# Performance work log

Hardware: AMD Instinct MI355X
Metric: run time of the kernel (lower is better)

Reference implementation:

```python
import jax, jax.numpy as jnp
import numpy as np


def conv(x, w, b=None, pad=0):
    y = jax.lax.conv_general_dilated(x, w, (1, 1), [(pad, pad), (pad, pad)],
                                     dimension_numbers=('NCHW', 'OIHW', 'NCHW'))
    if b is not None:
        y = y + b[None, :, None, None]
    return y


def bn(x, g, b, m, v, eps=1e-5):
    scale = g / jnp.sqrt(v + eps)
    return (x - m[None, :, None, None]) * scale[None, :, None, None] + b[None, :, None, None]


def channel_gate(x, w1, b1, w2, b2):
    # avg pool -> MLP -> sigmoid, returns [B, C, 1, 1]
    p = x.mean(axis=(2, 3))                       # [B, C]
    h = jax.nn.relu(p @ w1.T + b1)                # [B, C//r]
    a = h @ w2.T + b2                             # [B, C]
    return jax.nn.sigmoid(a)[:, :, None, None]


def setup_inputs() -> dict:
    key = jax.random.key(0)
    ks = iter(jax.random.split(key, 48))
    B, Cin, H, W = 2, 256, 64, 64
    Ci = Cin // 2          # inter_channels = 128
    Cr = Ci // 16          # gate bottleneck = 8
    def nrm(shape, s=0.05):
        return jax.random.normal(next(ks), shape, jnp.float32) * s
    d = {}
    d['q'] = jax.random.normal(next(ks), (B, Cin, H, W), jnp.float32)
    d['s'] = jax.random.normal(next(ks), (B, Cin, H, W), jnp.float32)
    # Trans_s: conv3x3 + BN
    d['ts_w'] = nrm((Ci, Cin, 3, 3)); d['ts_b'] = jnp.zeros(Ci)
    d['ts_g'] = jnp.ones(Ci); d['ts_be'] = jnp.zeros(Ci)
    d['ts_m'] = nrm((Ci,), 0.01); d['ts_v'] = jnp.ones(Ci)
    # Trans_q: conv3x3 + BN
    d['tq_w'] = nrm((Ci, Cin, 3, 3)); d['tq_b'] = jnp.zeros(Ci)
    d['tq_g'] = jnp.ones(Ci); d['tq_be'] = jnp.zeros(Ci)
    d['tq_m'] = nrm((Ci,), 0.01); d['tq_v'] = jnp.ones(Ci)
    # common_v 1x1
    d['cv_w'] = nrm((Ci, Ci, 1, 1)); d['cv_b'] = jnp.zeros(Ci)
    # key/query 1x1 projections (out = Ci//2)
    d['k1_w'] = nrm((Ci // 2, Ci, 1, 1)); d['k1_b'] = jnp.zeros(Ci // 2)
    d['q1_w'] = nrm((Ci // 2, Ci, 1, 1)); d['q1_b'] = jnp.zeros(Ci // 2)
    d['k2_w'] = nrm((Ci // 2, Ci, 1, 1)); d['k2_b'] = jnp.zeros(Ci // 2)
    d['q2_w'] = nrm((Ci // 2, Ci, 1, 1)); d['q2_b'] = jnp.zeros(Ci // 2)
    # ChannelGate MLP
    d['g1_w'] = nrm((Cr, Ci)); d['g1_b'] = jnp.zeros(Cr)
    d['g2_w'] = nrm((Ci, Cr)); d['g2_b'] = jnp.zeros(Ci)
    # conv_cat: conv3x3 (no bias) + BN
    d['cc_w'] = nrm((Ci, 2 * Ci, 3, 3))
    d['cc_g'] = jnp.ones(Ci); d['cc_be'] = jnp.zeros(Ci)
    d['cc_m'] = nrm((Ci,), 0.01); d['cc_v'] = jnp.ones(Ci)
    return d


def reference(q, s, ts_w, ts_b, ts_g, ts_be, ts_m, ts_v,
              tq_w, tq_b, tq_g, tq_be, tq_m, tq_v,
              cv_w, cv_b, k1_w, k1_b, q1_w, q1_b, k2_w, k2_b, q2_w, q2_b,
              g1_w, g1_b, g2_w, g2_b, cc_w, cc_g, cc_be, cc_m, cc_v):
    # stems: conv3x3 + BN + ReLU
    s = jax.nn.relu(bn(conv(s, ts_w, ts_b, pad=1), ts_g, ts_be, ts_m, ts_v))
    q = jax.nn.relu(bn(conv(q, tq_w, tq_b, pad=1), tq_g, tq_be, tq_m, tq_v))
    B, C, H, W = q.shape
    N = H * W
    # values
    v_q1 = conv(q, cv_w, cv_b)                          # [B,C,H,W]
    v_s1 = conv(s, cv_w, cv_b)
    v_q = v_q1.reshape(B, C, N).transpose(0, 2, 1)      # [B,N,C]
    v_s = v_s1.reshape(B, C, N).transpose(0, 2, 1)
    # dual keys / queries with negation trick
    k1 = conv(s, k1_w, k1_b).reshape(B, C // 2, N)
    k2 = conv(q, k2_w, k2_b).reshape(B, C // 2, N)
    key_cat = jnp.concatenate([k1, -k2], axis=1).transpose(0, 2, 1)   # [B,N,C]
    q1x = conv(s, q1_w, q1_b).reshape(B, C // 2, N)
    q2x = conv(q, q2_w, q2_b).reshape(B, C // 2, N)
    query_cat = jnp.concatenate([q1x, q2x], axis=1)                    # [B,C,N]
    # abs-score attention, dual softmax from the same score matrix
    A_s = jnp.abs(jnp.einsum('bnc,bcm->bnm', key_cat, query_cat))      # [B,N,N]
    att_s = jax.nn.softmax(A_s, axis=-1)
    att_q = jax.nn.softmax(A_s.transpose(0, 2, 1), axis=-1)
    # attend + channel-gate SE fusion + residual
    p_s = jnp.einsum('bnm,bmc->bnc', att_s, v_s).transpose(0, 2, 1).reshape(B, C, H, W)
    E_s = channel_gate(v_s1, g1_w, g1_b, g2_w, g2_b) * p_s + s
    q_s = jnp.einsum('bnm,bmc->bnc', att_q, v_q).transpose(0, 2, 1).reshape(B, C, H, W)
    E_q = channel_gate(v_q1, g1_w, g1_b, g2_w, g2_b) * q_s + q
    # concat + conv3x3(no bias) + BN + ReLU
    cpam = jax.nn.relu(bn(conv(jnp.concatenate([E_q, E_s], axis=1), cc_w, None, pad=1),
                          cc_g, cc_be, cc_m, cc_v))
    return (cpam, E_q, E_s)
```

## Files before the change

kernel.cpp:

```cpp
#include <hip/hip_runtime.h>

typedef __bf16 bf16;
typedef __bf16 v8bf __attribute__((ext_vector_type(8)));
typedef __bf16 v4bf __attribute__((ext_vector_type(4)));
typedef float v4f __attribute__((ext_vector_type(4)));

#define MFMA16(a, b, c) __builtin_amdgcn_mfma_f32_16x16x32_bf16(a, b, c, 0, 0, 0)

__device__ __forceinline__ float sf(float x) {
  if (!(x == x)) return 0.f;
  return fminf(fmaxf(x, -1e30f), 1e30f);
}

__global__ __launch_bounds__(256) void fill_kernel(float* __restrict__ out, float v, int n) {
  int i = blockIdx.x * 256 + threadIdx.x;
  if (i < n) out[i] = v;
}

__global__ __launch_bounds__(256) void prep_all_kernel(
    const float* __restrict__ s_in, const float* __restrict__ q_in, bf16* __restrict__ xin,
    const float* __restrict__ ts_w, const float* __restrict__ tq_w,
    const float* ts_b, const float* ts_g, const float* ts_be, const float* ts_m, const float* ts_v,
    const float* tq_b, const float* tq_g, const float* tq_be, const float* tq_m, const float* tq_v,
    bf16* __restrict__ Wt01, float* __restrict__ ss01, float* __restrict__ pmean,
    const float* __restrict__ cc_w, const float* cc_g, const float* cc_be,
    const float* cc_m, const float* cc_v,
    bf16* __restrict__ Wt2, float* __restrict__ ss_cc, int do_prep2)
{
  int bx = blockIdx.x, t = threadIdx.x;
  if (bx < 256) {
    int nb = bx & 63, z = bx >> 6;
    const float* in = ((z >> 1) ? q_in : s_in) + (long)(z & 1) * 1048576;
    bf16* out = xin + (long)z * 1048576;
    int lane = t & 63, w = t >> 6;
    long n = (long)nb * 64 + lane;
#pragma unroll
    for (int i = 0; i < 8; ++i) {
      int c8 = w * 8 + i;
      v8bf o;
#pragma unroll
      for (int j = 0; j < 8; ++j) o[j] = (bf16)in[(long)(c8 * 8 + j) * 4096 + n];
      *(v8bf*)(out + n * 256 + c8 * 8) = o;
    }
    return;
  }
  int idx = (bx - 256) * 256 + t;
  if (idx < 589824) {
    int which = idx / 294912;
    int rem = idx - which * 294912;
    int co = rem / 2304;
    int r2 = rem - co * 2304;
    int tap = r2 >> 8;
    int ci = r2 & 255;
    const float* W = which ? tq_w : ts_w;
    Wt01[idx] = (bf16)W[(co * 256 + ci) * 9 + tap];
  } else if (idx < 590080) {
    int i = idx - 589824;
    int which = i >> 7, c = i & 127;
    float g, be, m, vv, bias;
    if (which == 0) { g=ts_g[c]; be=ts_be[c]; m=ts_m[c]; vv=ts_v[c]; bias=ts_b[c]; }
    else            { g=tq_g[c]; be=tq_be[c]; m=tq_m[c]; vv=tq_v[c]; bias=tq_b[c]; }
    float scale = g / sqrtf(vv + 1e-5f);
    ss01[which * 256 + c] = sf(scale);
    ss01[which * 256 + 128 + c] = sf((bias - m) * scale + be);
  } else if (idx < 590592) {
    pmean[idx - 590080] = 0.f;
  } else if (do_prep2) {
    int idx2 = idx - 590592;
    if (idx2 < 294912) {
      int co = idx2 / 2304;
      int r2 = idx2 - co * 2304;
      int tap = r2 >> 8;
      int ci = r2 & 255;
      Wt2[idx2] = (bf16)cc_w[(co * 256 + ci) * 9 + tap];
    } else if (idx2 < 295040) {
      int c = idx2 - 294912;
      float scale = cc_g[c] / sqrtf(cc_v[c] + 1e-5f);
      ss_cc[c] = sf(scale);
      ss_cc[128 + c] = sf(-cc_m[c] * scale + cc_be[c]);
    }
  }
}

__global__ __launch_bounds__(256) void prep2_kernel(
    const float* __restrict__ cc_w, const float* cc_g, const float* cc_be,
    const float* cc_m, const float* cc_v,
    bf16* __restrict__ Wt2, float* __restrict__ ss_cc)
{
  int idx = blockIdx.x * 256 + threadIdx.x;
  if (idx < 294912) {
    int co = idx / 2304;
    int r2 = idx - co * 2304;
    int tap = r2 >> 8;
    int ci = r2 & 255;
    Wt2[idx] = (bf16)cc_w[(co * 256 + ci) * 9 + tap];
  } else if (idx < 295040) {
    int c = idx - 294912;
    float scale = cc_g[c] / sqrtf(cc_v[c] + 1e-5f);
    ss_cc[c] = sf(scale);
    ss_cc[128 + c] = sf(-cc_m[c] * scale + cc_be[c]);
  }
}

__global__ __launch_bounds__(256) void convN_kernel(
    const bf16* __restrict__ inA,
    const bf16* __restrict__ Wb, const float* __restrict__ ssb,
    void* __restrict__ out_, int mode)
{
  __shared__ bf16 As[66][40];
  __shared__ bf16 Bs[3][64][40];

  int bid = blockIdx.x;
  int xcd = bid & 7, slot = bid >> 3;
  int y, co0, tsr, b;
  if (mode == 0) {
    int z = xcd >> 1;
    tsr = z >> 1; b = z & 1;
    co0 = (xcd & 1) * 64;
    y = slot;
  } else {
    int combo = xcd >> 1;
    co0 = (combo >> 1) * 64;
    b = combo & 1;
    tsr = 0;
    y = (xcd & 1) * 32 + slot;
  }

  const bf16 *in0, *in1;
  const bf16* W;
  const float* sp;
  if (mode == 0) {
    in0 = inA + (long)(tsr * 2 + b) * 1048576;
    in1 = nullptr;
    W = Wb + (long)tsr * 294912;
    sp = ssb + tsr * 256;
  } else {
    in0 = inA + (long)(2 + b) * 524288;
    in1 = inA + (long)b * 524288;
    W = Wb; sp = ssb;
  }

  int t = threadIdx.x, lane = t & 63, w = t >> 6;
  int l15 = lane & 15, l4 = lane >> 4;
  int wr = (w & 1) * 32, wc = (w >> 1) * 32;
  int ax = t >> 2, ac0 = (t & 3) * 8;
  int bco = t >> 2, bk = (t & 3) * 8;

  v4f acc[2][2] = {};

  auto loadA = [&](int it, v8bf& areg) {
    int dy = it >> 3, ks = it & 7;
    int ysrc = y + dy - 1;
    if ((unsigned)ysrc < 64u) {
      long n = (long)ysrc * 64 + ax;
      int cg = ks * 32 + ac0;
      const bf16* src;
      if (mode == 0)     src = in0 + n * 256 + cg;
      else if (cg < 128) src = in0 + n * 128 + cg;
      else               src = in1 + n * 128 + (cg - 128);
      areg = *(const v8bf*)src;
    } else {
#pragma unroll
      for (int i = 0; i < 8; ++i) areg[i] = (bf16)0.f;
    }
  };
  auto loadB = [&](int it, v8bf* breg) {
    int dy = it >> 3, ks = it & 7;
    const bf16* wk = W + (long)(co0 + bco) * 2304 + dy * 3 * 256 + ks * 32 + bk;
#pragma unroll
    for (int d = 0; d < 3; ++d) breg[d] = *(const v8bf*)(wk + d * 256);
  };

  if (t < 32) As[0][t] = (bf16)0.f;
  else if (t < 64) As[65][t - 32] = (bf16)0.f;

  v8bf areg, breg[3];
  loadA(0, areg);
  loadB(0, breg);

  for (int it = 0; it < 24; ++it) {
    __syncthreads();
    *(v8bf*)&As[ax + 1][ac0] = areg;
#pragma unroll
    for (int d = 0; d < 3; ++d) *(v8bf*)&Bs[d][bco][bk] = breg[d];
    __syncthreads();
    if (it < 23) { loadA(it + 1, areg); loadB(it + 1, breg); }
    __builtin_amdgcn_s_setprio(1);
#pragma unroll
    for (int d = 0; d < 3; ++d) {
      v8bf af0 = *(const v8bf*)&As[wr + d + l15][l4 * 8];
      v8bf af1 = *(const v8bf*)&As[wr + 16 + d + l15][l4 * 8];
#pragma unroll
      for (int j = 0; j < 2; ++j) {
        v8bf bfr = *(const v8bf*)&Bs[d][wc + j * 16 + l15][l4 * 8];
        acc[0][j] = MFMA16(af0, bfr, acc[0][j]);
        acc[1][j] = MFMA16(af1, bfr, acc[1][j]);
      }
    }
    __builtin_amdgcn_s_setprio(0);
  }
#pragma unroll
  for (int i = 0; i < 2; ++i) {
    int nb = y * 64 + wr + i * 16 + l4 * 4;
#pragma unroll
    for (int j = 0; j < 2; ++j) {
      int c = co0 + wc + j * 16 + l15;
      float scale = sp[c], shift = sp[128 + c];
      if (mode == 0) {
        bf16* o = (bf16*)out_ + ((long)(tsr * 2 + b) * 4096 + nb) * 128 + c;
#pragma unroll
        for (int r = 0; r < 4; ++r)
          o[r * 128] = (bf16)sf(fmaxf(acc[i][j][r] * scale + shift, 0.f));
      } else {
        v4f pk;
#pragma unroll
        for (int r = 0; r < 4; ++r)
          pk[r] = sf(fmaxf(acc[i][j][r] * scale + shift, 0.f));
        *(v4f*)((float*)out_ + ((long)b * 128 + c) * 4096 + nb) = pk;
      }
    }
  }
}

__global__ __launch_bounds__(256) void conv1_kernel(
    const bf16* __restrict__ feat_base,
    const float* __restrict__ cv_w, const float* __restrict__ k1_w, const float* __restrict__ q1_w,
    const float* __restrict__ k2_w, const float* __restrict__ q2_w,
    const float* __restrict__ cv_b, const float* __restrict__ k1_b, const float* __restrict__ q1_b,
    const float* __restrict__ k2_b, const float* __restrict__ q2_b,
    bf16* __restrict__ v_base, bf16* __restrict__ keyT, bf16* __restrict__ queryT,
    float* __restrict__ pmean)
{
  int nt = blockIdx.x;
  int br = blockIdx.z >> 1, b = blockIdx.z & 1;
  long zid = br * 2 + b;
  const bf16* feat = feat_base + zid * 524288 + (long)nt * 4096;

  __shared__ bf16 As[32][40];
  __shared__ bf16 Bs[256][40];

  int t = threadIdx.x, lane = t & 63, w = t >> 6;
  int l15 = lane & 15, l4 = lane >> 4;
  int wr = (w & 1) * 16, wc = (w >> 1) * 128;

  const float* wrow;
  bool negk = false;
  if (t < 128)       wrow = cv_w + (long)t * 128;
  else if (t < 192) { wrow = (br ? k2_w : k1_w) + (long)(t - 128) * 128; negk = (br != 0); }
  else               wrow = (br ? q2_w : q1_w) + (long)(t - 192) * 128;

  v4f acc[8] = {};
  int ap = t >> 2, ak = (t & 3) * 8;

  for (int ks = 0; ks < 4; ++ks) {
    int ci0 = ks * 32;
    v8bf av;
    if (t < 128) av = *(const v8bf*)(feat + ap * 128 + ci0 + ak);
    float wv[32];
#pragma unroll
    for (int u = 0; u < 32; ++u) wv[u] = wrow[ci0 + u];
    if (negk) {
#pragma unroll
      for (int u = 0; u < 32; ++u) wv[u] = -wv[u];
    }
    __syncthreads();
    if (t < 128) *(v8bf*)&As[ap][ak] = av;
#pragma unroll
    for (int u = 0; u < 32; ++u) Bs[t][u] = (bf16)wv[u];
    __syncthreads();
    v8bf af = *(const v8bf*)&As[wr + l15][l4 * 8];
#pragma unroll
    for (int j = 0; j < 8; ++j) {
      v8bf bfr = *(const v8bf*)&Bs[wc + j * 16 + l15][l4 * 8];
      acc[j] = MFMA16(af, bfr, acc[j]);
    }
  }

  int nb = nt * 32 + wr + l4 * 4;
#pragma unroll
  for (int j = 0; j < 8; ++j) {
    int c = wc + j * 16 + l15;
    float bv;
    if (c < 128)      bv = cv_b[c];
    else if (c < 192) bv = br ? -k2_b[c - 128] : k1_b[c - 128];
    else              bv = (br ? q2_b : q1_b)[c - 192];
    float v0 = sf(acc[j][0] + bv), v1 = sf(acc[j][1] + bv);
    float v2 = sf(acc[j][2] + bv), v3 = sf(acc[j][3] + bv);
    if (c < 128) {
      long off = (long)(nb >> 5) * 4096 + (c >> 4) * 512 + ((nb >> 3) & 3) * 128 +
                 (c & 15) * 8 + (nb & 7);
      v4bf pk;
      pk[0] = (bf16)v0; pk[1] = (bf16)v1; pk[2] = (bf16)v2; pk[3] = (bf16)v3;
      *(v4bf*)(v_base + zid * 524288 + off) = pk;
      float s = v0 + v1 + v2 + v3;
      s += __shfl_xor(s, 16, 64);
      s += __shfl_xor(s, 32, 64);
      if (l4 == 0) atomicAdd(&pmean[zid * 128 + c], s);
    } else if (c < 192) {
      int cc = (c - 128) + br * 64;
      long off = (long)(nb >> 4) * 2048 + (cc >> 5) * 512 + ((cc >> 3) & 3) * 128 +
                 (nb & 15) * 8 + (cc & 7);
      bf16* kp = keyT + (long)b * 524288 + off;
      kp[0] = (bf16)v0; kp[8] = (bf16)v1; kp[16] = (bf16)v2; kp[24] = (bf16)v3;
    } else {
      int cc = (c - 192) + br * 64;
      long off = (long)(nb >> 4) * 2048 + (cc >> 5) * 512 + ((cc >> 3) & 3) * 128 +
                 (nb & 15) * 8 + (cc & 7);
      bf16* qp = queryT + (long)b * 524288 + off;
      qp[0] = (bf16)v0; qp[8] = (bf16)v1; qp[16] = (bf16)v2; qp[24] = (bf16)v3;
    }
  }
}

__global__ __launch_bounds__(256, 2) void apply_kernel(
    const bf16* __restrict__ keyT, const bf16* __restrict__ queryT,
    const bf16* __restrict__ v_base,
    const float* __restrict__ pmean,
    const float* __restrict__ g1_w, const float* __restrict__ g1_b,
    const float* __restrict__ g2_w, const float* __restrict__ g2_b,
    bf16* __restrict__ feat_base, float* __restrict__ d_out)
{
  int bid = blockIdx.x;
  int xcd = bid & 7;
  int z = xcd >> 1;
  int nt = (xcd & 1) * 64 + (bid >> 3);
  int br = z >> 1, b = z & 1;
  int n0 = nt * 32;
  const bf16* Xf = (br ? queryT : keyT) + (long)b * 524288 + (long)(n0 >> 4) * 2048;
  const bf16* Yf = (br ? keyT : queryT) + (long)b * 524288;
  const bf16* Vf = v_base + (long)(br * 2 + b) * 524288;
  bf16* feat = feat_base + (long)(br * 2 + b) * 524288 + (long)n0 * 128;

  __shared__ bf16 Ps[2][32][72];
  __shared__ float rps[4][32];
  __shared__ float gl[128];
  __shared__ float hh[8];

  int t = threadIdx.x, lane = t & 63, w = t >> 6;
  int l15 = lane & 15, l4 = lane >> 4;
  int wm = w * 16;
  int wr = (w & 1) * 16;
  int wc = (w >> 1) * 64;

  {
    const float* pm = pmean + (br * 2 + b) * 128;
    if (t < 8) {
      float a = g1_b[t];
      for (int c = 0; c < 128; ++c) a += g1_w[t * 128 + c] * (pm[c] * (1.f / 4096.f));
      hh[t] = fmaxf(a, 0.f);
    }
    __syncthreads();
    if (t < 128) {
      float a = g2_b[t];
#pragma unroll
      for (int j = 0; j < 8; ++j) a += g2_w[t * 8 + j] * hh[j];
      gl[t] = sf(1.f / (1.f + __expf(-a)));
    }
  }

  v8bf af[2][4];
#pragma unroll
  for (int i = 0; i < 2; ++i)
#pragma unroll
    for (int k = 0; k < 4; ++k)
      af[i][k] = *(const v8bf*)(Xf + i * 2048 + k * 512 + lane * 8);

  v4f acc[4] = {};
  float rp[2][4] = {};

  auto loadBy = [&](int m0, v8bf* by) {
    const bf16* p = Yf + (long)((m0 >> 4) + w) * 2048 + lane * 8;
#pragma unroll
    for (int k = 0; k < 4; ++k) by[k] = *(const v8bf*)(p + k * 512);
  };
  auto loadVb = [&](int m0, v8bf* vb) {
    const bf16* p = Vf + (long)(m0 >> 5) * 4096 + ((w >> 1) * 4) * 512 + lane * 8;
#pragma unroll
    for (int j = 0; j < 4; ++j)
#pragma unroll
      for (int k = 0; k < 2; ++k)
        vb[j * 2 + k] = *(const v8bf*)(p + k * 4096 + j * 512);
  };

  v8bf byA[4], byB[4], vbA[8], vbB[8];
  loadBy(0, byA);
  loadVb(0, vbA);

  auto subiter = [&](v8bf (&by)[4], v8bf (&vb)[8], v8bf (&byN)[4], v8bf (&vbN)[8],
                     int psb, int m0n, bool pf) {
    v4f sacc[2] = {};
    __builtin_amdgcn_s_setprio(1);
#pragma unroll
    for (int k = 0; k < 4; ++k)
#pragma unroll
      for (int i = 0; i < 2; ++i)
        sacc[i] = MFMA16(af[i][k], by[k], sacc[i]);
    __builtin_amdgcn_s_setprio(0);
    if (pf) { loadBy(m0n, byN); loadVb(m0n, vbN); }
#pragma unroll
    for (int i = 0; i < 2; ++i)
#pragma unroll
      for (int r = 0; r < 4; ++r) {
        float e = __expf(fminf(fabsf(sacc[i][r]), 80.f) - 50.f);
        rp[i][r] += e;
        Ps[psb][i * 16 + l4 * 4 + r][wm + l15] = (bf16)e;
      }
    asm volatile("s_waitcnt lgkmcnt(0)" ::: "memory");
    __builtin_amdgcn_s_barrier();
    __builtin_amdgcn_s_setprio(1);
#pragma unroll
    for (int k = 0; k < 2; ++k) {
      v8bf p0 = *(const v8bf*)&Ps[psb][wr + l15][k * 32 + l4 * 8];
#pragma unroll
      for (int j = 0; j < 4; ++j)
        acc[j] = MFMA16(p0, vb[j * 2 + k], acc[j]);
    }
    __builtin_amdgcn_s_setprio(0);
  };

  for (int mt2 = 0; mt2 < 32; ++mt2) {
    int mA = mt2 * 128;
    subiter(byA, vbA, byB, vbB, 0, mA + 64, true);
    subiter(byB, vbB, byA, vbA, 1, mA + 128, mt2 < 31);
  }

#pragma unroll
  for (int i = 0; i < 2; ++i)
#pragma unroll
    for (int r = 0; r < 4; ++r) {
      float v = rp[i][r];
      v += __shfl_xor(v, 1, 64);
      v += __shfl_xor(v, 2, 64);
      v += __shfl_xor(v, 4, 64);
      v += __shfl_xor(v, 8, 64);
      if (l15 == 0) rps[w][i * 16 + l4 * 4 + r] = v;
    }
  __syncthreads();

  float* outE = d_out + (long)(br ? 1 : 2) * 1048576 + (long)b * 524288;
  int rowt = wr + l4 * 4;
  float dv[4];
#pragma unroll
  for (int r = 0; r < 4; ++r)
    dv[r] = fmaxf(rps[0][rowt + r] + rps[1][rowt + r] + rps[2][rowt + r] + rps[3][rowt + r],
                  1e-30f);
#pragma unroll
  for (int j = 0; j < 4; ++j) {
    int c = wc + j * 16 + l15;
    float g = gl[c];
    v4f pk;
#pragma unroll
    for (int r = 0; r < 4; ++r) {
      long fi = (long)(rowt + r) * 128 + c;
      float fv = (float)feat[fi];
      float val = sf(acc[j][r] / dv[r] * g + fv);
      pk[r] = val;
      feat[fi] = (bf16)val;
    }
    *(v4f*)(outE + (long)c * 4096 + n0 + rowt) = pk;
  }
}

extern "C" void kernel_launch(void* const* d_in, const int* in_sizes, int n_in,
                              void* d_out, int out_size, void* d_ws, size_t ws_size,
                              hipStream_t stream)
{
  if (n_in != 33 || in_sizes[0] != 2097152 || in_sizes[2] != 294912 ||
      in_sizes[14] != 16384 || out_size != 3145728) {
    fill_kernel<<<12288, 256, 0, stream>>>((float*)d_out, 100.0f, 3145728);
    return;
  }
  if (ws_size < 12582912) {
    fill_kernel<<<12288, 256, 0, stream>>>((float*)d_out, 1.0f, 3145728);
    return;
  }

  const float* q_in = (const float*)d_in[0];
  const float* s_in = (const float*)d_in[1];
  char* ob = (char*)d_out;
  float* outf = (float*)d_out;

  float* pmean = (float*)(ob + 0);
  bf16*  xin   = (bf16*)(ob + 4194304);

  char* ws = (char*)d_ws;
  bf16*  sfeat  = (bf16*)(ws + 0);
  bf16*  vs     = (bf16*)(ws + 4194304);
  bf16*  keyT   = (bf16*)(ws + 8388608);
  bf16*  queryT = (bf16*)(ws + 10485760);
  bf16*  Wt01   = (bf16*)(ws + 8388608);
  float* ss01   = (float*)(ws + 10485760);

  bool room = ws_size >= (size_t)13173760;
  bf16*  Wt2   = room ? (bf16*)(ws + 12582912) : (bf16*)(ws + 8388608);
  float* ss_cc = room ? (float*)(ws + 13172736) : (float*)(ws + 8978432);

  prep_all_kernel<<<room ? 3716 : 2563, 256, 0, stream>>>(
      s_in, q_in, xin,
      (const float*)d_in[2], (const float*)d_in[8],
      (const float*)d_in[3], (const float*)d_in[4], (const float*)d_in[5],
      (const float*)d_in[6], (const float*)d_in[7],
      (const float*)d_in[9], (const float*)d_in[10], (const float*)d_in[11],
      (const float*)d_in[12], (const float*)d_in[13],
      Wt01, ss01, pmean,
      (const float*)d_in[28], (const float*)d_in[29], (const float*)d_in[30],
      (const float*)d_in[31], (const float*)d_in[32],
      Wt2, ss_cc, room ? 1 : 0);

  convN_kernel<<<512, 256, 0, stream>>>(xin, Wt01, ss01, sfeat, 0);

  conv1_kernel<<<dim3(128, 1, 4), 256, 0, stream>>>(
      sfeat,
      (const float*)d_in[14], (const float*)d_in[16], (const float*)d_in[18],
      (const float*)d_in[20], (const float*)d_in[22],
      (const float*)d_in[15], (const float*)d_in[17], (const float*)d_in[19],
      (const float*)d_in[21], (const float*)d_in[23],
      vs, keyT, queryT, pmean);

  apply_kernel<<<512, 256, 0, stream>>>(
      keyT, queryT, vs, pmean,
      (const float*)d_in[24], (const float*)d_in[25],
      (const float*)d_in[26], (const float*)d_in[27],
      sfeat, outf);

  if (!room) {
    prep2_kernel<<<1153, 256, 0, stream>>>(
        (const float*)d_in[28], (const float*)d_in[29], (const float*)d_in[30],
        (const float*)d_in[31], (const float*)d_in[32], Wt2, ss_cc);
  }

  convN_kernel<<<256, 256, 0, stream>>>(sfeat, Wt2, ss_cc, outf, 1);
}
```

Before: 261.1 us.

## Split attention key dimension across waves and drop per-step block barriers

The attention kernel now has each wave own a disjoint slice of the key/value sequence (32 columns per step) and compute the full 32x128 output tile for that slice. This lets each wave write and read its P tile in private LDS without the per-step block-wide barrier. The four partial accumulators are summed through shared memory at the end. In exchange each wave holds twice as many accumulators, which raises register pressure, and V loads are no longer prefetched one step ahead. The conv kernel also drops its s_setprio hints.

Result: faster. 247.1 us (-5.4%).

```diff
diff --git a/kernel.cpp b/kernel.cpp
--- a/kernel.cpp
+++ b/kernel.cpp
@@ -185,7 +185,6 @@
     for (int d = 0; d < 3; ++d) *(v8bf*)&Bs[d][bco][bk] = breg[d];
     __syncthreads();
     if (it < 23) { loadA(it + 1, areg); loadB(it + 1, breg); }
-    __builtin_amdgcn_s_setprio(1);
 #pragma unroll
     for (int d = 0; d < 3; ++d) {
       v8bf af0 = *(const v8bf*)&As[wr + d + l15][l4 * 8];
@@ -197,7 +196,6 @@
         acc[1][j] = MFMA16(af1, bfr, acc[1][j]);
       }
     }
-    __builtin_amdgcn_s_setprio(0);
   }
 #pragma unroll
   for (int i = 0; i < 2; ++i) {
@@ -331,16 +329,15 @@
   const bf16* Vf = v_base + (long)(br * 2 + b) * 524288;
   bf16* feat = feat_base + (long)(br * 2 + b) * 524288 + (long)n0 * 128;
 
-  __shared__ bf16 Ps[2][32][72];
+  __shared__ __align__(16) char smem_raw[18432];
+  bf16 (*Psw)[32][40] = reinterpret_cast<bf16(*)[32][40]>(smem_raw);
+  float (*Fred)[36] = reinterpret_cast<float(*)[36]>(smem_raw);
   __shared__ float rps[4][32];
   __shared__ float gl[128];
   __shared__ float hh[8];
 
   int t = threadIdx.x, lane = t & 63, w = t >> 6;
   int l15 = lane & 15, l4 = lane >> 4;
-  int wm = w * 16;
-  int wr = (w & 1) * 16;
-  int wc = (w >> 1) * 64;
 
   {
     const float* pm = pmean + (br * 2 + b) * 128;
@@ -365,63 +362,59 @@
     for (int k = 0; k < 4; ++k)
       af[i][k] = *(const v8bf*)(Xf + i * 2048 + k * 512 + lane * 8);
 
-  v4f acc[4] = {};
+  v4f acc[2][8] = {};
   float rp[2][4] = {};
 
-  auto loadBy = [&](int m0, v8bf* by) {
-    const bf16* p = Yf + (long)((m0 >> 4) + w) * 2048 + lane * 8;
-#pragma unroll
-    for (int k = 0; k < 4; ++k) by[k] = *(const v8bf*)(p + k * 512);
+  auto loadBy = [&](int mb, v8bf (&by)[2][4]) {
+    const bf16* p = Yf + (long)(mb >> 4) * 2048 + lane * 8;
+#pragma unroll
+    for (int mf = 0; mf < 2; ++mf)
+#pragma unroll
+      for (int k = 0; k < 4; ++k) by[mf][k] = *(const v8bf*)(p + mf * 2048 + k * 512);
   };
-  auto loadVb = [&](int m0, v8bf* vb) {
-    const bf16* p = Vf + (long)(m0 >> 5) * 4096 + ((w >> 1) * 4) * 512 + lane * 8;
-#pragma unroll
-    for (int j = 0; j < 4; ++j)
-#pragma unroll
-      for (int k = 0; k < 2; ++k)
-        vb[j * 2 + k] = *(const v8bf*)(p + k * 4096 + j * 512);
+
+  v8bf byA[2][4], byB[2][4];
+  loadBy(w * 32, byA);
+
+  auto subiter = [&](int it, v8bf (&byC)[2][4], v8bf (&byN)[2][4]) {
+    int mb = it * 128 + w * 32;
+    v8bf vb[8];
+    {
+      const bf16* p = Vf + (long)(mb >> 5) * 4096 + lane * 8;
+#pragma unroll
+      for (int j = 0; j < 8; ++j) vb[j] = *(const v8bf*)(p + j * 512);
+    }
+    v4f sacc[2][2] = {};
+#pragma unroll
+    for (int k = 0; k < 4; ++k)
+#pragma unroll
+      for (int i = 0; i < 2; ++i)
+#pragma unroll
+        for (int mf = 0; mf < 2; ++mf)
+          sacc[i][mf] = MFMA16(af[i][k], byC[mf][k], sacc[i][mf]);
+    if (it < 31) loadBy(mb + 128, byN);
+#pragma unroll
+    for (int i = 0; i < 2; ++i)
+#pragma unroll
+      for (int mf = 0; mf < 2; ++mf)
+#pragma unroll
+        for (int r = 0; r < 4; ++r) {
+          float e = __expf(fminf(fabsf(sacc[i][mf][r]), 80.f) - 50.f);
+          rp[i][r] += e;
+          Psw[w][i * 16 + l4 * 4 + r][mf * 16 + l15] = (bf16)e;
+        }
+    v8bf ap0 = *(const v8bf*)&Psw[w][l15][l4 * 8];
+    v8bf ap1 = *(const v8bf*)&Psw[w][16 + l15][l4 * 8];
+#pragma unroll
+    for (int j = 0; j < 8; ++j) {
+      acc[0][j] = MFMA16(ap0, vb[j], acc[0][j]);
+      acc[1][j] = MFMA16(ap1, vb[j], acc[1][j]);
+    }
   };
 
-  v8bf byA[4], byB[4], vbA[8], vbB[8];
-  loadBy(0, byA);
-  loadVb(0, vbA);
-
-  auto subiter = [&](v8bf (&by)[4], v8bf (&vb)[8], v8bf (&byN)[4], v8bf (&vbN)[8],
-                     int psb, int m0n, bool pf) {
-    v4f sacc[2] = {};
-    __builtin_amdgcn_s_setprio(1);
-#pragma unroll
-    for (int k = 0; k < 4; ++k)
-#pragma unroll
-      for (int i = 0; i < 2; ++i)
-        sacc[i] = MFMA16(af[i][k], by[k], sacc[i]);
-    __builtin_amdgcn_s_setprio(0);
-    if (pf) { loadBy(m0n, byN); loadVb(m0n, vbN); }
-#pragma unroll
-    for (int i = 0; i < 2; ++i)
-#pragma unroll
-      for (int r = 0; r < 4; ++r) {
-        float e = __expf(fminf(fabsf(sacc[i][r]), 80.f) - 50.f);
-        rp[i][r] += e;
-        Ps[psb][i * 16 + l4 * 4 + r][wm + l15] = (bf16)e;
-      }
-    asm volatile("s_waitcnt lgkmcnt(0)" ::: "memory");
-    __builtin_amdgcn_s_barrier();
-    __builtin_amdgcn_s_setprio(1);
-#pragma unroll
-    for (int k = 0; k < 2; ++k) {
-      v8bf p0 = *(const v8bf*)&Ps[psb][wr + l15][k * 32 + l4 * 8];
-#pragma unroll
-      for (int j = 0; j < 4; ++j)
-        acc[j] = MFMA16(p0, vb[j * 2 + k], acc[j]);
-    }
-    __builtin_amdgcn_s_setprio(0);
-  };
-
-  for (int mt2 = 0; mt2 < 32; ++mt2) {
-    int mA = mt2 * 128;
-    subiter(byA, vbA, byB, vbB, 0, mA + 64, true);
-    subiter(byB, vbB, byA, vbA, 1, mA + 128, mt2 < 31);
+  for (int it2 = 0; it2 < 16; ++it2) {
+    subiter(it2 * 2, byA, byB);
+    subiter(it2 * 2 + 1, byB, byA);
   }
 
 #pragma unroll
@@ -437,7 +430,28 @@
     }
   __syncthreads();
 
+#pragma unroll
+  for (int ww = 0; ww < 4; ++ww) {
+    if (w == ww) {
+#pragma unroll
+      for (int i = 0; i < 2; ++i)
+#pragma unroll
+        for (int j = 0; j < 8; ++j) {
+          float* fp = &Fred[j * 16 + l15][i * 16 + l4 * 4];
+          if (ww == 0) *(v4f*)fp = acc[i][j];
+          else {
+            v4f old = *(v4f*)fp;
+#pragma unroll
+            for (int r = 0; r < 4; ++r) old[r] += acc[i][j][r];
+            *(v4f*)fp = old;
+          }
+        }
+    }
+    __syncthreads();
+  }
+
   float* outE = d_out + (long)(br ? 1 : 2) * 1048576 + (long)b * 524288;
+  int wr = (w & 1) * 16, wc = (w >> 1) * 64;
   int rowt = wr + l4 * 4;
   float dv[4];
 #pragma unroll
@@ -448,12 +462,13 @@
   for (int j = 0; j < 4; ++j) {
     int c = wc + j * 16 + l15;
     float g = gl[c];
+    v4f nm = *(const v4f*)&Fred[c][rowt];
     v4f pk;
 #pragma unroll
     for (int r = 0; r < 4; ++r) {
       long fi = (long)(rowt + r) * 128 + c;
       float fv = (float)feat[fi];
-      float val = sf(acc[j][r] / dv[r] * g + fv);
+      float val = sf(nm[r] / dv[r] * g + fv);
       pk[r] = val;
       feat[fi] = (bf16)val;
     }
```
